# Performance work log

Hardware: AMD Instinct MI355X
Metric: run time of the kernel (lower is better)

The kernel has to match this reference:

```python
import jax, jax.numpy as jnp
import numpy as np

BETA = 0.9
TH = 1.0  # snn.Leaky default threshold
SPARSITY = 0.5


@jax.custom_vjp
def spike(x):
    # Heaviside spike; surrogate (atan, alpha=2) gradient as in snntorch default
    return (x > 0).astype(x.dtype)

def _spike_fwd(x):
    return spike(x), x

def _spike_bwd(x, g):
    return (g / (1.0 + (jnp.pi * x) ** 2),)

spike.defvjp(_spike_fwd, _spike_bwd)


def setup_inputs() -> dict:
    key = jax.random.key(0)
    ks = jax.random.split(key, 6)
    T, B, NIN, NH, NOUT = 50, 512, 784, 1000, 10

    def mk_w(k, o, i):
        k1, k2 = jax.random.split(k)
        w = jax.random.normal(k1, (o, i), jnp.float32) * (1.0 / np.sqrt(i))
        mask = (jax.random.uniform(k2, (o, i)) > SPARSITY).astype(jnp.float32)
        return w * mask

    x = jax.random.normal(ks[0], (T, B, NIN), jnp.float32)
    return dict(
        x=x,
        W0=mk_w(ks[1], NH, NIN), b0=jnp.zeros((NH,), jnp.float32),
        W1=mk_w(ks[2], NH, NH), b1=jnp.zeros((NH,), jnp.float32),
        W2=mk_w(ks[3], NH, NH), b2=jnp.zeros((NH,), jnp.float32),
        W3=mk_w(ks[4], NOUT, NH), b3=jnp.zeros((NOUT,), jnp.float32),
    )


def reference(x, W0, b0, W1, b1, W2, b2, W3, b3):
    params = ((W0, b0), (W1, b1), (W2, b2), (W3, b3))
    B = x.shape[1]
    mems0 = tuple(jnp.zeros((B, W.shape[0]), x.dtype) for W, _ in params)

    def step(mems, xt):
        inp = xt
        new_mems, spks = [], []
        for (W, b), m in zip(params, mems):
            cur = inp @ W.T + b
            # snntorch Leaky (reset_mechanism='subtract'):
            # reset from previous mem (detached), then mem = beta*mem + I - reset*th
            reset = jax.lax.stop_gradient((m > TH).astype(x.dtype))
            m_new = BETA * m + cur - reset * TH
            s = spike(m_new - TH)
            new_mems.append(m_new)
            spks.append(s)
            inp = s
        return tuple(new_mems), (tuple(spks), tuple(new_mems))

    _, (spk_rec, mem_rec) = jax.lax.scan(step, mems0, x)
    # spk_rec/mem_rec: tuples of [T, B, dim] arrays per layer
    return (*spk_rec, *mem_rec)
```

## Files before the change

kernel.cpp:

```cpp
#include <hip/hip_runtime.h>


typedef int int4v  __attribute__((ext_vector_type(4)));
typedef int int16v __attribute__((ext_vector_type(16)));

#define XSCALE 68719476736.0
#define WSCALE 1099511627776.0
#define MT 25600

__global__ void wsplit_i8(const float* __restrict__ W, signed char* __restrict__ out,
                          int Nreal, int Npad, int K, int Kpad)
{
    int idx = blockIdx.x * blockDim.x + threadIdx.x;
    int total = Npad * Kpad;
    if (idx >= total) return;
    int n = idx / Kpad, k = idx - n * Kpad;
    long long v = 0;
    if (n < Nreal && k < K) v = __double2ll_rn((double)W[(size_t)n * K + k] * WSCALE);
    size_t plane = (size_t)total;
#pragma unroll
    for (int p = 0; p < 4; ++p) {
        int d = (int)(v & 255); if (d > 127) d -= 256;
        out[p * plane + idx] = (signed char)d;
        v = (v - d) >> 8;
    }
    out[4 * plane + idx] = (signed char)v;
}

__global__ void xsplit_all(const float* __restrict__ x, signed char* __restrict__ out)
{
    int idx = blockIdx.x * blockDim.x + threadIdx.x;
    if (idx >= MT * 832) return;
    int row = idx / 832, k = idx - row * 832;
    long long v = 0;
    if (k < 784) v = __double2ll_rn((double)x[(size_t)row * 784 + k] * XSCALE);
    const size_t plane = (size_t)MT * 832;
    signed char* o = out + idx;
#pragma unroll
    for (int p = 0; p < 4; ++p) {
        int d = (int)(v & 255); if (d > 127) d -= 256;
        o[p * plane] = (signed char)d;
        v = (v - d) >> 8;
    }
    o[4 * plane] = (signed char)v;
}

template<int NA, int KP, int CS>
__global__ __launch_bounds__(256)
void gemm32(const signed char* __restrict__ Ap, size_t planeA,
            const signed char* __restrict__ Wp, size_t planeW,
            double* __restrict__ curout)
{
    __shared__ __align__(16) signed char Wld[5 * 64 * 80];
    __shared__ __align__(16) signed char Ald[NA * 64 * 80];
    constexpr int NIT = KP / 64;

    const int tid = threadIdx.x;
    const int l   = tid & 63;
    const int w   = tid >> 6;
    const int wm  = (w & 1) * 32;
    const int wn  = (w >> 1) * 32;
    const int r32 = l & 31;
    const int h   = l >> 5;

    const int bm = blockIdx.y * 64;
    const int bn = blockIdx.x * 64;

    const int srow = tid >> 2;
    const int sc   = (tid & 3) * 16;

    const signed char* ag = Ap + (size_t)(bm + srow) * KP + sc;
    const signed char* wg = Wp + (size_t)(bn + srow) * KP + sc;

    int4v Ar[NA], Wr[5];
#pragma unroll
    for (int p = 0; p < 5; ++p)  Wr[p] = *(const int4v*)(wg + p * planeW);
#pragma unroll
    for (int p = 0; p < NA; ++p) Ar[p] = *(const int4v*)(ag + p * planeA);

    int16v acc[5];
#pragma unroll
    for (int s = 0; s < 5; ++s)
#pragma unroll
        for (int r = 0; r < 16; ++r) acc[s][r] = 0;

    for (int it = 0; it < NIT; ++it) {
        __syncthreads();
#pragma unroll
        for (int p = 0; p < 5; ++p)
            *(int4v*)&Wld[(p * 64 + srow) * 80 + sc] = Wr[p];
#pragma unroll
        for (int p = 0; p < NA; ++p)
            *(int4v*)&Ald[(p * 64 + srow) * 80 + sc] = Ar[p];
        __syncthreads();

        if (it + 1 < NIT) {
            int kb = (it + 1) * 64;
#pragma unroll
            for (int p = 0; p < 5; ++p)
                Wr[p] = *(const int4v*)(wg + kb + p * planeW);
#pragma unroll
            for (int p = 0; p < NA; ++p)
                Ar[p] = *(const int4v*)(ag + kb + p * planeA);
        }

#pragma unroll
        for (int k2 = 0; k2 < 2; ++k2) {
            const int off = k2 * 32 + 16 * h;
            if constexpr (NA == 5) {
                int4v af[5], bq[5];
#pragma unroll
                for (int p = 0; p < 5; ++p)
                    af[p] = *(const int4v*)&Ald[(p * 64 + wm + r32) * 80 + off];
#pragma unroll
                for (int q = 0; q < 5; ++q)
                    bq[q] = *(const int4v*)&Wld[(q * 64 + wn + r32) * 80 + off];
#pragma unroll
                for (int q = 0; q < 5; ++q)
#pragma unroll
                    for (int p = 0; p < 5; ++p)
                        if (p + q >= 4)
                            acc[p + q - 4] = __builtin_amdgcn_mfma_i32_32x32x32_i8(
                                af[p], bq[q], acc[p + q - 4], 0, 0, 0);
            } else {
                int4v a0 = *(const int4v*)&Ald[(wm + r32) * 80 + off];
#pragma unroll
                for (int q = 0; q < 5; ++q) {
                    int4v bq = *(const int4v*)&Wld[(q * 64 + wn + r32) * 80 + off];
                    acc[q] = __builtin_amdgcn_mfma_i32_32x32x32_i8(a0, bq, acc[q], 0, 0, 0);
                }
            }
        }
    }

    const int col = bn + wn + r32;
    if (col < CS) {
#pragma unroll
        for (int reg = 0; reg < 16; ++reg) {
            int row = bm + wm + (reg & 3) + 8 * (reg >> 2) + 4 * h;
            double v = (double)acc[4][reg];
            v = v * 256.0 + (double)acc[3][reg];
            v = v * 256.0 + (double)acc[2][reg];
            v = v * 256.0 + (double)acc[1][reg];
            v = v * 256.0 + (double)acc[0][reg];
            curout[(size_t)row * CS + col] = v * (NA == 5 ? 0x1p-44 : 0x1p-40);
        }
    }
}

template<int KP>
__global__ __launch_bounds__(256)
void gemm32w(const signed char* __restrict__ Asp,
             const signed char* __restrict__ Wp, size_t planeW,
             double* __restrict__ curout)
{
    __shared__ __align__(16) signed char Wld[5 * 64 * 80];
    __shared__ __align__(16) signed char Ald[128 * 80];
    constexpr int NIT = KP / 64;

    const int tid = threadIdx.x;
    const int l   = tid & 63;
    const int w   = tid >> 6;
    const int wm  = (w & 1) * 64;
    const int wn  = (w >> 1) * 32;
    const int r32 = l & 31;
    const int h   = l >> 5;

    const int bm = blockIdx.y * 128;
    const int bn = blockIdx.x * 64;

    const int srA = tid >> 1;
    const int scA = (tid & 1) * 32;
    const int srW = tid >> 2;
    const int scW = (tid & 3) * 16;

    const signed char* ag = Asp + (size_t)(bm + srA) * KP + scA;
    const signed char* wg = Wp  + (size_t)(bn + srW) * KP + scW;

    int4v Ar0 = *(const int4v*)(ag);
    int4v Ar1 = *(const int4v*)(ag + 16);
    int4v Wr[5];
#pragma unroll
    for (int p = 0; p < 5; ++p) Wr[p] = *(const int4v*)(wg + p * planeW);

    int16v acc[2][5];
#pragma unroll
    for (int mi = 0; mi < 2; ++mi)
#pragma unroll
        for (int s = 0; s < 5; ++s)
#pragma unroll
            for (int r = 0; r < 16; ++r) acc[mi][s][r] = 0;

    for (int it = 0; it < NIT; ++it) {
        __syncthreads();
#pragma unroll
        for (int p = 0; p < 5; ++p)
            *(int4v*)&Wld[(p * 64 + srW) * 80 + scW] = Wr[p];
        *(int4v*)&Ald[srA * 80 + scA]      = Ar0;
        *(int4v*)&Ald[srA * 80 + scA + 16] = Ar1;
        __syncthreads();

        if (it + 1 < NIT) {
            int kb = (it + 1) * 64;
            Ar0 = *(const int4v*)(ag + kb);
            Ar1 = *(const int4v*)(ag + kb + 16);
#pragma unroll
            for (int p = 0; p < 5; ++p)
                Wr[p] = *(const int4v*)(wg + kb + p * planeW);
        }

#pragma unroll
        for (int k2 = 0; k2 < 2; ++k2) {
            const int off = k2 * 32 + 16 * h;
            int4v bq[5];
#pragma unroll
            for (int q = 0; q < 5; ++q)
                bq[q] = *(const int4v*)&Wld[(q * 64 + wn + r32) * 80 + off];
#pragma unroll
            for (int mi = 0; mi < 2; ++mi) {
                int4v a0 = *(const int4v*)&Ald[(wm + mi * 32 + r32) * 80 + off];
#pragma unroll
                for (int q = 0; q < 5; ++q)
                    acc[mi][q] = __builtin_amdgcn_mfma_i32_32x32x32_i8(
                        a0, bq[q], acc[mi][q], 0, 0, 0);
            }
        }
    }

    const int col = bn + wn + r32;
#pragma unroll
    for (int mi = 0; mi < 2; ++mi)
#pragma unroll
        for (int reg = 0; reg < 16; ++reg) {
            int row = bm + wm + mi * 32 + (reg & 3) + 8 * (reg >> 2) + 4 * h;
            double v = (double)acc[mi][4][reg];
            v = v * 256.0 + (double)acc[mi][3][reg];
            v = v * 256.0 + (double)acc[mi][2][reg];
            v = v * 256.0 + (double)acc[mi][1][reg];
            v = v * 256.0 + (double)acc[mi][0][reg];
            curout[(size_t)row * 1024 + col] = v * 0x1p-40;
        }
}

__global__ __launch_bounds__(256)
void if_update(const double* __restrict__ cur, const float* __restrict__ bias,
               float* __restrict__ spk, float* __restrict__ mem,
               signed char* __restrict__ spk_i8)
{
    int idx = blockIdx.x * blockDim.x + threadIdx.x;
    if (idx >= 512 * 500) return;
    int row = idx / 500, col = (idx - row * 500) * 2;
    double mp0 = 0.0, mp1 = 0.0;
    double bs0 = (double)bias[col], bs1 = (double)bias[col + 1];
    for (int t = 0; t < 50; ++t) {
        double2 c = *(const double2*)&cur[((size_t)t * 512 + row) * 1024 + col];
        double rst0 = (mp0 > 1.0) ? 1.0 : 0.0;
        double rst1 = (mp1 > 1.0) ? 1.0 : 0.0;
        double mn0 = 0.9 * mp0 + (c.x + bs0) - rst0;
        double mn1 = 0.9 * mp1 + (c.y + bs1) - rst1;
        int s0 = (mn0 > 1.0) ? 1 : 0;
        int s1 = (mn1 > 1.0) ? 1 : 0;
        size_t o = ((size_t)t * 512 + row) * 1000 + col;
        *(float2*)&spk[o] = make_float2((float)s0, (float)s1);
        *(float2*)&mem[o] = make_float2((float)mn0, (float)mn1);
        *(short*)&spk_i8[((size_t)t * 512 + row) * 1024 + col] =
            (short)(s0 | (s1 << 8));
        mp0 = mn0; mp1 = mn1;
    }
}

__global__ __launch_bounds__(256)
void if3_kernel(const double* __restrict__ cur3, const float* __restrict__ bias,
                float* __restrict__ spk3, float* __restrict__ mem3)
{
    int idx = blockIdx.x * blockDim.x + threadIdx.x;
    if (idx >= 5120) return;
    int brow = idx / 10, col = idx - brow * 10;
    double bs = (double)bias[col];
    double mp = 0.0;
    for (int t = 0; t < 50; ++t) {
        double c   = cur3[((size_t)t * 512 + brow) * 16 + col] + bs;
        double rst = (mp > 1.0) ? 1.0 : 0.0;
        double mn  = 0.9 * mp + c - rst;
        size_t o   = (size_t)t * 5120 + (size_t)brow * 10 + col;
        spk3[o] = (mn > 1.0) ? 1.0f : 0.0f;
        mem3[o] = (float)mn;
        mp = mn;
    }
}

extern "C" void kernel_launch(void* const* d_in, const int* in_sizes, int n_in,
                              void* d_out, int out_size, void* d_ws, size_t ws_size,
                              hipStream_t stream)
{
    const float* x  = (const float*)d_in[0];
    const float* W0 = (const float*)d_in[1];
    const float* b0 = (const float*)d_in[2];
    const float* W1 = (const float*)d_in[3];
    const float* b1 = (const float*)d_in[4];
    const float* W2 = (const float*)d_in[5];
    const float* b2 = (const float*)d_in[6];
    const float* W3 = (const float*)d_in[7];
    const float* b3 = (const float*)d_in[8];
    float* out = (float*)d_out;

    const int T = 50;
    const size_t LNH = (size_t)512 * 1000;
    const size_t LNO = (size_t)512 * 10;

    float* spk0 = out;
    float* spk1 = spk0 + (size_t)T * LNH;
    float* spk2 = spk1 + (size_t)T * LNH;
    float* spk3 = spk2 + (size_t)T * LNH;
    float* mem0 = spk3 + (size_t)T * LNO;
    float* mem1 = mem0 + (size_t)T * LNH;
    float* mem2 = mem1 + (size_t)T * LNH;
    float* mem3 = mem2 + (size_t)T * LNH;

    double* cur = (double*)d_ws;
    signed char* W0d = (signed char*)(cur + (size_t)MT * 1024);
    signed char* W1d = W0d + (size_t)5 * 1024 * 832;
    signed char* W2d = W1d + (size_t)5 * 1024 * 1024;
    signed char* W3d = W2d + (size_t)5 * 1024 * 1024;
    signed char* xsb = W3d + (size_t)5 * 64 * 1024;
    signed char* sp0 = xsb + (size_t)5 * MT * 832;
    signed char* sp1 = sp0 + (size_t)MT * 1024;
    signed char* sp2 = sp1 + (size_t)MT * 1024;

    hipMemsetAsync(sp0, 0, (size_t)3 * MT * 1024, stream);

    wsplit_i8<<<(1024 * 832  + 255) / 256, 256, 0, stream>>>(W0, W0d, 1000, 1024, 784,  832);
    wsplit_i8<<<(1024 * 1024 + 255) / 256, 256, 0, stream>>>(W1, W1d, 1000, 1024, 1000, 1024);
    wsplit_i8<<<(1024 * 1024 + 255) / 256, 256, 0, stream>>>(W2, W2d, 1000, 1024, 1000, 1024);
    wsplit_i8<<<(64 * 1024   + 255) / 256, 256, 0, stream>>>(W3, W3d, 10,   64,   1000, 1024);

    xsplit_all<<<(MT * 832 + 255) / 256, 256, 0, stream>>>(x, xsb);

    const size_t plA0 = (size_t)MT * 832;
    const size_t plW0 = (size_t)1024 * 832;
    const size_t plWH = (size_t)1024 * 1024;
    const size_t plW3 = (size_t)64 * 1024;

    dim3 blk(256);
    dim3 g0(16, MT / 64);
    dim3 gW(16, MT / 128);
    dim3 g3(1, MT / 64);

    gemm32<5, 832, 1024><<<g0, blk, 0, stream>>>(xsb, plA0, W0d, plW0, cur);
    if_update<<<1000, 256, 0, stream>>>(cur, b0, spk0, mem0, sp0);
    gemm32w<1024><<<gW, blk, 0, stream>>>(sp0, W1d, plWH, cur);
    if_update<<<1000, 256, 0, stream>>>(cur, b1, spk1, mem1, sp1);
    gemm32w<1024><<<gW, blk, 0, stream>>>(sp1, W2d, plWH, cur);
    if_update<<<1000, 256, 0, stream>>>(cur, b2, spk2, mem2, sp2);
    gemm32<1, 1024, 16><<<g3, blk, 0, stream>>>(sp2, 0, W3d, plW3, cur);
    if3_kernel<<<20, 256, 0, stream>>>(cur, b3, spk3, mem3);
}
```

Before: 1.060 ms.

## Double-buffer LDS in hidden-layer GEMM and fold spike padding zeroing into update

The hidden-layer int8 GEMM now uses two LDS buffers. Each iteration computes on one buffer while storing the prefetched next tile into the other, which cuts the loop from two barriers to one. Separately, the 3x25.6MB memset of the padded int8 spike buffers is removed. Instead, the LIF update kernel launches extra threads that write zeros to the pad columns 1000-1023. LDS use doubles, which may reduce occupancy.

Result: no change. 1.061 ms (+0.1%).

```diff
diff --git a/kernel.cpp b/kernel.cpp
--- a/kernel.cpp
+++ b/kernel.cpp
@@ -154,8 +154,8 @@
              const signed char* __restrict__ Wp, size_t planeW,
              double* __restrict__ curout)
 {
-    __shared__ __align__(16) signed char Wld[5 * 64 * 80];
-    __shared__ __align__(16) signed char Ald[128 * 80];
+    __shared__ __align__(16) signed char Wld[2][5 * 64 * 80];
+    __shared__ __align__(16) signed char Ald[2][128 * 80];
     constexpr int NIT = KP / 64;
 
     const int tid = threadIdx.x;
@@ -182,6 +182,19 @@
     int4v Wr[5];
 #pragma unroll
     for (int p = 0; p < 5; ++p) Wr[p] = *(const int4v*)(wg + p * planeW);
+#pragma unroll
+    for (int p = 0; p < 5; ++p)
+        *(int4v*)&Wld[0][(p * 64 + srW) * 80 + scW] = Wr[p];
+    *(int4v*)&Ald[0][srA * 80 + scA]      = Ar0;
+    *(int4v*)&Ald[0][srA * 80 + scA + 16] = Ar1;
+    if (NIT > 1) {
+        Ar0 = *(const int4v*)(ag + 64);
+        Ar1 = *(const int4v*)(ag + 64 + 16);
+#pragma unroll
+        for (int p = 0; p < 5; ++p)
+            Wr[p] = *(const int4v*)(wg + 64 + p * planeW);
+    }
+    __syncthreads();
 
     int16v acc[2][5];
 #pragma unroll
@@ -192,22 +205,7 @@
             for (int r = 0; r < 16; ++r) acc[mi][s][r] = 0;
 
     for (int it = 0; it < NIT; ++it) {
-        __syncthreads();
-#pragma unroll
-        for (int p = 0; p < 5; ++p)
-            *(int4v*)&Wld[(p * 64 + srW) * 80 + scW] = Wr[p];
-        *(int4v*)&Ald[srA * 80 + scA]      = Ar0;
-        *(int4v*)&Ald[srA * 80 + scA + 16] = Ar1;
-        __syncthreads();
-
-        if (it + 1 < NIT) {
-            int kb = (it + 1) * 64;
-            Ar0 = *(const int4v*)(ag + kb);
-            Ar1 = *(const int4v*)(ag + kb + 16);
-#pragma unroll
-            for (int p = 0; p < 5; ++p)
-                Wr[p] = *(const int4v*)(wg + kb + p * planeW);
-        }
+        const int cur = it & 1;
 
 #pragma unroll
         for (int k2 = 0; k2 < 2; ++k2) {
@@ -215,15 +213,33 @@
             int4v bq[5];
 #pragma unroll
             for (int q = 0; q < 5; ++q)
-                bq[q] = *(const int4v*)&Wld[(q * 64 + wn + r32) * 80 + off];
+                bq[q] = *(const int4v*)&Wld[cur][(q * 64 + wn + r32) * 80 + off];
 #pragma unroll
             for (int mi = 0; mi < 2; ++mi) {
-                int4v a0 = *(const int4v*)&Ald[(wm + mi * 32 + r32) * 80 + off];
+                int4v a0 = *(const int4v*)&Ald[cur][(wm + mi * 32 + r32) * 80 + off];
 #pragma unroll
                 for (int q = 0; q < 5; ++q)
                     acc[mi][q] = __builtin_amdgcn_mfma_i32_32x32x32_i8(
                         a0, bq[q], acc[mi][q], 0, 0, 0);
             }
+        }
+
+        if (it + 1 < NIT) {
+            const int nxt = cur ^ 1;
+#pragma unroll
+            for (int p = 0; p < 5; ++p)
+                *(int4v*)&Wld[nxt][(p * 64 + srW) * 80 + scW] = Wr[p];
+            *(int4v*)&Ald[nxt][srA * 80 + scA]      = Ar0;
+            *(int4v*)&Ald[nxt][srA * 80 + scA + 16] = Ar1;
+            if (it + 2 < NIT) {
+                int kb = (it + 2) * 64;
+                Ar0 = *(const int4v*)(ag + kb);
+                Ar1 = *(const int4v*)(ag + kb + 16);
+#pragma unroll
+                for (int p = 0; p < 5; ++p)
+                    Wr[p] = *(const int4v*)(wg + kb + p * planeW);
+            }
+            __syncthreads();
         }
     }
 
@@ -248,8 +264,13 @@
                signed char* __restrict__ spk_i8)
 {
     int idx = blockIdx.x * blockDim.x + threadIdx.x;
-    if (idx >= 512 * 500) return;
-    int row = idx / 500, col = (idx - row * 500) * 2;
+    if (idx >= 512 * 512) return;
+    int row = idx >> 9, col = (idx & 511) * 2;
+    if (col >= 1000) {
+        for (int t = 0; t < 50; ++t)
+            *(short*)&spk_i8[((size_t)t * 512 + row) * 1024 + col] = 0;
+        return;
+    }
     double mp0 = 0.0, mp1 = 0.0;
     double bs0 = (double)bias[col], bs1 = (double)bias[col + 1];
     for (int t = 0; t < 50; ++t) {
@@ -327,8 +348,6 @@
     signed char* sp1 = sp0 + (size_t)MT * 1024;
     signed char* sp2 = sp1 + (size_t)MT * 1024;
 
-    hipMemsetAsync(sp0, 0, (size_t)3 * MT * 1024, stream);
-
     wsplit_i8<<<(1024 * 832  + 255) / 256, 256, 0, stream>>>(W0, W0d, 1000, 1024, 784,  832);
     wsplit_i8<<<(1024 * 1024 + 255) / 256, 256, 0, stream>>>(W1, W1d, 1000, 1024, 1000, 1024);
     wsplit_i8<<<(1024 * 1024 + 255) / 256, 256, 0, stream>>>(W2, W2d, 1000, 1024, 1000, 1024);
@@ -347,11 +366,11 @@
     dim3 g3(1, MT / 64);
 
     gemm32<5, 832, 1024><<<g0, blk, 0, stream>>>(xsb, plA0, W0d, plW0, cur);
-    if_update<<<1000, 256, 0, stream>>>(cur, b0, spk0, mem0, sp0);
+    if_update<<<1024, 256, 0, stream>>>(cur, b0, spk0, mem0, sp0);
     gemm32w<1024><<<gW, blk, 0, stream>>>(sp0, W1d, plWH, cur);
-    if_update<<<1000, 256, 0, stream>>>(cur, b1, spk1, mem1, sp1);
+    if_update<<<1024, 256, 0, stream>>>(cur, b1, spk1, mem1, sp1);
     gemm32w<1024><<<gW, blk, 0, stream>>>(sp1, W2d, plWH, cur);
-    if_update<<<1000, 256, 0, stream>>>(cur, b2, spk2, mem2, sp2);
+    if_update<<<1024, 256, 0, stream>>>(cur, b2, spk2, mem2, sp2);
     gemm32<1, 1024, 16><<<g3, blk, 0, stream>>>(sp2, 0, W3d, plW3, cur);
     if3_kernel<<<20, 256, 0, stream>>>(cur, b3, spk3, mem3);
 }
```

## Fuse input digit-splitting into layer-0 GEMM and drop spike buffer memset

Applied to the files above, without the earlier changes.

Removes the separate xsplit_all pass that wrote five int8 digit planes of x to global memory, and instead computes the digits on the fly inside a dedicated layer-0 GEMM from float loads. The if_update kernel now zero-fills the padded spike columns itself, so the up-front memset of the spike buffers is gone. W1 and W2 splitting is merged into a single launch. This cuts a large write-and-read of the digit planes and a couple of launches, at the cost of extra ALU work (double conversions) in the GEMM's load path, which is recomputed once per column block.

Result: slower. 1.206 ms (+13.8%).

```diff
diff --git a/kernel.cpp b/kernel.cpp
--- a/kernel.cpp
+++ b/kernel.cpp
@@ -27,33 +27,71 @@
     out[4 * plane + idx] = (signed char)v;
 }
 
-__global__ void xsplit_all(const float* __restrict__ x, signed char* __restrict__ out)
-{
+__global__ void wsplit_i8x2(const float* __restrict__ Wa, signed char* __restrict__ oa,
+                            const float* __restrict__ Wb, signed char* __restrict__ ob)
+{
+    const float* W = blockIdx.y ? Wb : Wa;
+    signed char* out = blockIdx.y ? ob : oa;
     int idx = blockIdx.x * blockDim.x + threadIdx.x;
-    if (idx >= MT * 832) return;
-    int row = idx / 832, k = idx - row * 832;
+    const int total = 1024 * 1024;
+    if (idx >= total) return;
+    int n = idx >> 10, k = idx & 1023;
     long long v = 0;
-    if (k < 784) v = __double2ll_rn((double)x[(size_t)row * 784 + k] * XSCALE);
-    const size_t plane = (size_t)MT * 832;
-    signed char* o = out + idx;
+    if (n < 1000 && k < 1000) v = __double2ll_rn((double)W[(size_t)n * 1000 + k] * WSCALE);
+    size_t plane = (size_t)total;
 #pragma unroll
     for (int p = 0; p < 4; ++p) {
         int d = (int)(v & 255); if (d > 127) d -= 256;
-        o[p * plane] = (signed char)d;
+        out[p * plane + idx] = (signed char)d;
         v = (v - d) >> 8;
     }
-    o[4 * plane] = (signed char)v;
-}
-
-template<int NA, int KP, int CS>
+    out[4 * plane + idx] = (signed char)v;
+}
+
+__device__ __forceinline__ void digit16(const float* __restrict__ xr, int k0,
+                                        int4v (&D)[5])
+{
+    float xv[16];
+    if (k0 + 16 <= 784) {
+#pragma unroll
+        for (int q = 0; q < 4; ++q) {
+            float4 f = *(const float4*)(xr + k0 + q * 4);
+            xv[q * 4 + 0] = f.x; xv[q * 4 + 1] = f.y;
+            xv[q * 4 + 2] = f.z; xv[q * 4 + 3] = f.w;
+        }
+    } else {
+#pragma unroll
+        for (int j = 0; j < 16; ++j) xv[j] = 0.f;
+    }
+    unsigned pk[5][4];
+#pragma unroll
+    for (int p = 0; p < 5; ++p)
+#pragma unroll
+        for (int q = 0; q < 4; ++q) pk[p][q] = 0;
+#pragma unroll
+    for (int j = 0; j < 16; ++j) {
+        long long v = __double2ll_rn((double)xv[j] * XSCALE);
+#pragma unroll
+        for (int p = 0; p < 4; ++p) {
+            int d = (int)(v & 255); if (d > 127) d -= 256;
+            pk[p][j >> 2] |= (unsigned)(d & 255) << ((j & 3) * 8);
+            v = (v - d) >> 8;
+        }
+        pk[4][j >> 2] |= (unsigned)((int)v & 255) << ((j & 3) * 8);
+    }
+#pragma unroll
+    for (int p = 0; p < 5; ++p)
+        D[p] = (int4v){(int)pk[p][0], (int)pk[p][1], (int)pk[p][2], (int)pk[p][3]};
+}
+
 __global__ __launch_bounds__(256)
-void gemm32(const signed char* __restrict__ Ap, size_t planeA,
-            const signed char* __restrict__ Wp, size_t planeW,
-            double* __restrict__ curout)
-{
+void gemm32_l0(const float* __restrict__ x,
+               const signed char* __restrict__ Wp, size_t planeW,
+               double* __restrict__ curout)
+{
+    constexpr int KP = 832, NIT = 13;
     __shared__ __align__(16) signed char Wld[5 * 64 * 80];
-    __shared__ __align__(16) signed char Ald[NA * 64 * 80];
-    constexpr int NIT = KP / 64;
+    __shared__ __align__(16) signed char Ald[5 * 64 * 80];
 
     const int tid = threadIdx.x;
     const int l   = tid & 63;
@@ -69,14 +107,101 @@
     const int srow = tid >> 2;
     const int sc   = (tid & 3) * 16;
 
+    const float* xr = x + (size_t)(bm + srow) * 784;
+    const signed char* wg = Wp + (size_t)(bn + srow) * KP + sc;
+
+    int4v Dr[5], Wr[5];
+#pragma unroll
+    for (int p = 0; p < 5; ++p) Wr[p] = *(const int4v*)(wg + p * planeW);
+    digit16(xr, sc, Dr);
+
+    int16v acc[5];
+#pragma unroll
+    for (int s = 0; s < 5; ++s)
+#pragma unroll
+        for (int r = 0; r < 16; ++r) acc[s][r] = 0;
+
+    for (int it = 0; it < NIT; ++it) {
+        __syncthreads();
+#pragma unroll
+        for (int p = 0; p < 5; ++p) {
+            *(int4v*)&Wld[(p * 64 + srow) * 80 + sc] = Wr[p];
+            *(int4v*)&Ald[(p * 64 + srow) * 80 + sc] = Dr[p];
+        }
+        __syncthreads();
+
+        if (it + 1 < NIT) {
+            int kb = (it + 1) * 64;
+#pragma unroll
+            for (int p = 0; p < 5; ++p)
+                Wr[p] = *(const int4v*)(wg + kb + p * planeW);
+            digit16(xr, kb + sc, Dr);
+        }
+
+#pragma unroll
+        for (int k2 = 0; k2 < 2; ++k2) {
+            const int off = k2 * 32 + 16 * h;
+            int4v af[5], bq[5];
+#pragma unroll
+            for (int p = 0; p < 5; ++p)
+                af[p] = *(const int4v*)&Ald[(p * 64 + wm + r32) * 80 + off];
+#pragma unroll
+            for (int q = 0; q < 5; ++q)
+                bq[q] = *(const int4v*)&Wld[(q * 64 + wn + r32) * 80 + off];
+#pragma unroll
+            for (int q = 0; q < 5; ++q)
+#pragma unroll
+                for (int p = 0; p < 5; ++p)
+                    if (p + q >= 4)
+                        acc[p + q - 4] = __builtin_amdgcn_mfma_i32_32x32x32_i8(
+                            af[p], bq[q], acc[p + q - 4], 0, 0, 0);
+        }
+    }
+
+    const int col = bn + wn + r32;
+#pragma unroll
+    for (int reg = 0; reg < 16; ++reg) {
+        int row = bm + wm + (reg & 3) + 8 * (reg >> 2) + 4 * h;
+        double v = (double)acc[4][reg];
+        v = v * 256.0 + (double)acc[3][reg];
+        v = v * 256.0 + (double)acc[2][reg];
+        v = v * 256.0 + (double)acc[1][reg];
+        v = v * 256.0 + (double)acc[0][reg];
+        curout[(size_t)row * 1024 + col] = v * 0x1p-44;
+    }
+}
+
+template<int KP, int CS>
+__global__ __launch_bounds__(256)
+void gemm32(const signed char* __restrict__ Ap,
+            const signed char* __restrict__ Wp, size_t planeW,
+            double* __restrict__ curout)
+{
+    __shared__ __align__(16) signed char Wld[5 * 64 * 80];
+    __shared__ __align__(16) signed char Ald[64 * 80];
+    constexpr int NIT = KP / 64;
+
+    const int tid = threadIdx.x;
+    const int l   = tid & 63;
+    const int w   = tid >> 6;
+    const int wm  = (w & 1) * 32;
+    const int wn  = (w >> 1) * 32;
+    const int r32 = l & 31;
+    const int h   = l >> 5;
+
+    const int bm = blockIdx.y * 64;
+    const int bn = blockIdx.x * 64;
+
+    const int srow = tid >> 2;
+    const int sc   = (tid & 3) * 16;
+
     const signed char* ag = Ap + (size_t)(bm + srow) * KP + sc;
     const signed char* wg = Wp + (size_t)(bn + srow) * KP + sc;
 
-    int4v Ar[NA], Wr[5];
-#pragma unroll
-    for (int p = 0; p < 5; ++p)  Wr[p] = *(const int4v*)(wg + p * planeW);
-#pragma unroll
-    for (int p = 0; p < NA; ++p) Ar[p] = *(const int4v*)(ag + p * planeA);
+    int4v Ar, Wr[5];
+#pragma unroll
+    for (int p = 0; p < 5; ++p) Wr[p] = *(const int4v*)(wg + p * planeW);
+    Ar = *(const int4v*)ag;
 
     int16v acc[5];
 #pragma unroll
@@ -89,9 +214,7 @@
 #pragma unroll
         for (int p = 0; p < 5; ++p)
             *(int4v*)&Wld[(p * 64 + srow) * 80 + sc] = Wr[p];
-#pragma unroll
-        for (int p = 0; p < NA; ++p)
-            *(int4v*)&Ald[(p * 64 + srow) * 80 + sc] = Ar[p];
+        *(int4v*)&Ald[srow * 80 + sc] = Ar;
         __syncthreads();
 
         if (it + 1 < NIT) {
@@ -99,36 +222,17 @@
 #pragma unroll
             for (int p = 0; p < 5; ++p)
                 Wr[p] = *(const int4v*)(wg + kb + p * planeW);
-#pragma unroll
-            for (int p = 0; p < NA; ++p)
-                Ar[p] = *(const int4v*)(ag + kb + p * planeA);
+            Ar = *(const int4v*)(ag + kb);
         }
 
 #pragma unroll
         for (int k2 = 0; k2 < 2; ++k2) {
             const int off = k2 * 32 + 16 * h;
-            if constexpr (NA == 5) {
-                int4v af[5], bq[5];
-#pragma unroll
-                for (int p = 0; p < 5; ++p)
-                    af[p] = *(const int4v*)&Ald[(p * 64 + wm + r32) * 80 + off];
-#pragma unroll
-                for (int q = 0; q < 5; ++q)
-                    bq[q] = *(const int4v*)&Wld[(q * 64 + wn + r32) * 80 + off];
-#pragma unroll
-                for (int q = 0; q < 5; ++q)
-#pragma unroll
-                    for (int p = 0; p < 5; ++p)
-                        if (p + q >= 4)
-                            acc[p + q - 4] = __builtin_amdgcn_mfma_i32_32x32x32_i8(
-                                af[p], bq[q], acc[p + q - 4], 0, 0, 0);
-            } else {
-                int4v a0 = *(const int4v*)&Ald[(wm + r32) * 80 + off];
-#pragma unroll
-                for (int q = 0; q < 5; ++q) {
-                    int4v bq = *(const int4v*)&Wld[(q * 64 + wn + r32) * 80 + off];
-                    acc[q] = __builtin_amdgcn_mfma_i32_32x32x32_i8(a0, bq, acc[q], 0, 0, 0);
-                }
+            int4v a0 = *(const int4v*)&Ald[(wm + r32) * 80 + off];
+#pragma unroll
+            for (int q = 0; q < 5; ++q) {
+                int4v bq = *(const int4v*)&Wld[(q * 64 + wn + r32) * 80 + off];
+                acc[q] = __builtin_amdgcn_mfma_i32_32x32x32_i8(a0, bq, acc[q], 0, 0, 0);
             }
         }
     }
@@ -143,7 +247,7 @@
             v = v * 256.0 + (double)acc[2][reg];
             v = v * 256.0 + (double)acc[1][reg];
             v = v * 256.0 + (double)acc[0][reg];
-            curout[(size_t)row * CS + col] = v * (NA == 5 ? 0x1p-44 : 0x1p-40);
+            curout[(size_t)row * CS + col] = v * 0x1p-40;
         }
     }
 }
@@ -248,8 +352,13 @@
                signed char* __restrict__ spk_i8)
 {
     int idx = blockIdx.x * blockDim.x + threadIdx.x;
-    if (idx >= 512 * 500) return;
-    int row = idx / 500, col = (idx - row * 500) * 2;
+    if (idx >= 512 * 512) return;
+    int row = idx >> 9, col = (idx & 511) * 2;
+    if (col >= 1000) {
+        for (int t = 0; t < 50; ++t)
+            *(short*)&spk_i8[((size_t)t * 512 + row) * 1024 + col] = 0;
+        return;
+    }
     double mp0 = 0.0, mp1 = 0.0;
     double bs0 = (double)bias[col], bs1 = (double)bias[col + 1];
     for (int t = 0; t < 50; ++t) {
@@ -322,21 +431,14 @@
     signed char* W1d = W0d + (size_t)5 * 1024 * 832;
     signed char* W2d = W1d + (size_t)5 * 1024 * 1024;
     signed char* W3d = W2d + (size_t)5 * 1024 * 1024;
-    signed char* xsb = W3d + (size_t)5 * 64 * 1024;
-    signed char* sp0 = xsb + (size_t)5 * MT * 832;
+    signed char* sp0 = W3d + (size_t)5 * 64 * 1024;
     signed char* sp1 = sp0 + (size_t)MT * 1024;
     signed char* sp2 = sp1 + (size_t)MT * 1024;
 
-    hipMemsetAsync(sp0, 0, (size_t)3 * MT * 1024, stream);
-
-    wsplit_i8<<<(1024 * 832  + 255) / 256, 256, 0, stream>>>(W0, W0d, 1000, 1024, 784,  832);
-    wsplit_i8<<<(1024 * 1024 + 255) / 256, 256, 0, stream>>>(W1, W1d, 1000, 1024, 1000, 1024);
-    wsplit_i8<<<(1024 * 1024 + 255) / 256, 256, 0, stream>>>(W2, W2d, 1000, 1024, 1000, 1024);
-    wsplit_i8<<<(64 * 1024   + 255) / 256, 256, 0, stream>>>(W3, W3d, 10,   64,   1000, 1024);
-
-    xsplit_all<<<(MT * 832 + 255) / 256, 256, 0, stream>>>(x, xsb);
-
-    const size_t plA0 = (size_t)MT * 832;
+    wsplit_i8<<<(1024 * 832 + 255) / 256, 256, 0, stream>>>(W0, W0d, 1000, 1024, 784, 832);
+    wsplit_i8x2<<<dim3((1024 * 1024 + 255) / 256, 2), 256, 0, stream>>>(W1, W1d, W2, W2d);
+    wsplit_i8<<<(64 * 1024 + 255) / 256, 256, 0, stream>>>(W3, W3d, 10, 64, 1000, 1024);
+
     const size_t plW0 = (size_t)1024 * 832;
     const size_t plWH = (size_t)1024 * 1024;
     const size_t plW3 = (size_t)64 * 1024;
@@ -346,12 +448,12 @@
     dim3 gW(16, MT / 128);
     dim3 g3(1, MT / 64);
 
-    gemm32<5, 832, 1024><<<g0, blk, 0, stream>>>(xsb, plA0, W0d, plW0, cur);
-    if_update<<<1000, 256, 0, stream>>>(cur, b0, spk0, mem0, sp0);
+    gemm32_l0<<<g0, blk, 0, stream>>>(x, W0d, plW0, cur);
+    if_update<<<1024, 256, 0, stream>>>(cur, b0, spk0, mem0, sp0);
     gemm32w<1024><<<gW, blk, 0, stream>>>(sp0, W1d, plWH, cur);
-    if_update<<<1000, 256, 0, stream>>>(cur, b1, spk1, mem1, sp1);
+    if_update<<<1024, 256, 0, stream>>>(cur, b1, spk1, mem1, sp1);
     gemm32w<1024><<<gW, blk, 0, stream>>>(sp1, W2d, plWH, cur);
-    if_update<<<1000, 256, 0, stream>>>(cur, b2, spk2, mem2, sp2);
-    gemm32<1, 1024, 16><<<g3, blk, 0, stream>>>(sp2, 0, W3d, plW3, cur);
+    if_update<<<1024, 256, 0, stream>>>(cur, b2, spk2, mem2, sp2);
+    gemm32<1024, 16><<<g3, blk, 0, stream>>>(sp2, W3d, plW3, cur);
     if3_kernel<<<20, 256, 0, stream>>>(cur, b3, spk3, mem3);
 }
```
